# Optimization experiments

Measured on AMD Instinct MI355X. Metric: run time of the kernel, lower is better.

## Reference

```python
import jax, jax.numpy as jnp
import numpy as np

D_MODEL = 768; N_LAYER = 4; D_STATE = 64; D_CONV = 4; EXPAND = 2; HEADDIM = 64
D_INNER = EXPAND * D_MODEL          # 1536
NHEADS = D_INNER // HEADDIM         # 24
CONV_DIM = D_INNER + 2 * D_STATE    # 1664
D_IN_PROJ = 2 * D_INNER + 2 * D_STATE + NHEADS  # 3224
VOCAB = 50257; EPS = 1e-5


def _ln(x, w, b):
    m = x.mean(-1, keepdims=True)
    v = ((x - m) ** 2).mean(-1, keepdims=True)
    return (x - m) * jax.lax.rsqrt(v + EPS) * w + b


def _silu(x):
    return x * jax.nn.sigmoid(x)


def _mamba2(x, W_in, conv_w, conv_b, dt_bias, A_log, Dp, rms_w, W_out):
    # x: [B, L, d_model]
    Bsz, L, _ = x.shape
    zxbcdt = x @ W_in.T                                   # [B,L,D_IN_PROJ]
    z = zxbcdt[..., :D_INNER]
    xBC = zxbcdt[..., D_INNER:D_INNER + CONV_DIM]
    dt = zxbcdt[..., D_INNER + CONV_DIM:]                 # [B,L,H]
    # causal depthwise conv over time
    xc = jnp.transpose(xBC, (0, 2, 1))                    # [B,C,L]
    xc = jax.lax.conv_general_dilated(
        xc, conv_w[:, None, :], (1,), [(D_CONV - 1, 0)],
        dimension_numbers=('NCH', 'OIH', 'NCH'), feature_group_count=CONV_DIM)
    xBC = _silu(jnp.transpose(xc, (0, 2, 1)) + conv_b)
    xh = xBC[..., :D_INNER].reshape(Bsz, L, NHEADS, HEADDIM)
    Bc = xBC[..., D_INNER:D_INNER + D_STATE]              # [B,L,N]
    Cc = xBC[..., D_INNER + D_STATE:]                     # [B,L,N]
    dt = jax.nn.softplus(dt + dt_bias)                    # [B,L,H]
    dA = jnp.exp(dt * (-jnp.exp(A_log)))                  # [B,L,H]

    def step(h, inp):
        dA_t, dt_t, x_t, B_t, C_t = inp
        h = dA_t[:, :, None, None] * h + (dt_t[:, :, None] * x_t)[..., None] * B_t[:, None, None, :]
        return h, jnp.einsum('bhpn,bn->bhp', h, C_t)

    tm = lambda a: jnp.moveaxis(a, 1, 0)  # time-major
    h0 = jnp.zeros((Bsz, NHEADS, HEADDIM, D_STATE), x.dtype)
    _, y = jax.lax.scan(step, h0, (tm(dA), tm(dt), tm(xh), tm(Bc), tm(Cc)))
    y = jnp.moveaxis(y, 0, 1) + Dp[:, None] * xh          # [B,L,H,P]
    y = y.reshape(Bsz, L, D_INNER) * _silu(z)             # gate
    y = y * jax.lax.rsqrt((y * y).mean(-1, keepdims=True) + EPS) * rms_w
    return y @ W_out.T


def setup_inputs() -> dict:
    key = jax.random.key(0)
    ks = jax.random.split(key, 16)
    B, L = 1, 1024
    idx = jax.random.randint(ks[0], (B, L), 0, VOCAB)
    targets = jax.random.randint(ks[1], (B, L), 0, VOCAB)
    s = 0.02
    emb = jax.random.normal(ks[2], (VOCAB, D_MODEL), jnp.float32) * s
    ln_w = jnp.ones((N_LAYER, D_MODEL)); ln_b = jnp.zeros((N_LAYER, D_MODEL))
    W_in = jax.random.normal(ks[3], (N_LAYER, D_IN_PROJ, D_MODEL), jnp.float32) * s
    conv_w = jax.random.normal(ks[4], (N_LAYER, CONV_DIM, D_CONV), jnp.float32) * 0.1
    conv_b = jnp.zeros((N_LAYER, CONV_DIM))
    dt_bias = jnp.log(jnp.expm1(jax.random.uniform(ks[5], (N_LAYER, NHEADS), minval=0.001, maxval=0.1)))
    A_log = jnp.log(jax.random.uniform(ks[6], (N_LAYER, NHEADS), minval=1.0, maxval=16.0))
    Dp = jnp.ones((N_LAYER, NHEADS))
    rms_w = jnp.ones((N_LAYER, D_INNER))
    W_out = jax.random.normal(ks[7], (N_LAYER, D_MODEL, D_INNER), jnp.float32) * s
    lnf_w = jnp.ones((D_MODEL,)); lnf_b = jnp.zeros((D_MODEL,))
    return {"idx": idx, "targets": targets, "emb": emb, "ln_w": ln_w, "ln_b": ln_b,
            "W_in": W_in, "conv_w": conv_w, "conv_b": conv_b, "dt_bias": dt_bias,
            "A_log": A_log, "Dp": Dp, "rms_w": rms_w, "W_out": W_out,
            "lnf_w": lnf_w, "lnf_b": lnf_b}


def reference(idx, targets, emb, ln_w, ln_b, W_in, conv_w, conv_b, dt_bias,
              A_log, Dp, rms_w, W_out, lnf_w, lnf_b):
    x = emb[idx]                                          # [B,L,D]
    for i in range(N_LAYER):
        x = x + _mamba2(_ln(x, ln_w[i], ln_b[i]), W_in[i], conv_w[i], conv_b[i],
                        dt_bias[i], A_log[i], Dp[i], rms_w[i], W_out[i])
    x = _ln(x, lnf_w, lnf_b)
    logits = x @ emb.T                                    # tied head
    logp = jax.nn.log_softmax(logits, axis=-1)
    loss = -jnp.take_along_axis(logp, targets[..., None], axis=-1).mean()
    return logits, loss
```

## Files before the change

### kernel.cpp

```cpp
#include <hip/hip_runtime.h>
#include <hip/hip_bf16.h>
#include <math.h>

#define SL     1024
#define DMODEL 768
#define NLAYER 4
#define NSTATE 64
#define HEADDIM 64
#define DINNER 1536
#define NHEADS 24
#define CONVDIM 1664
#define DINPROJ 3224
#define VOCABN 50257

typedef __attribute__((ext_vector_type(8))) short short8;
typedef __attribute__((ext_vector_type(4))) short short4v;
typedef __attribute__((ext_vector_type(4))) float f32x4;

__device__ __forceinline__ short f2bf(float f) {
    unsigned int u = __builtin_bit_cast(unsigned int, f);
    u += 0x7fffu + ((u >> 16) & 1u);
    return (short)(u >> 16);
}

#define AS1 __attribute__((address_space(1)))
#define AS3 __attribute__((address_space(3)))
__device__ __forceinline__ void gl2lds16(const void* g, void* l) {
    __builtin_amdgcn_global_load_lds((const AS1 unsigned int*)g,
                                     (AS3 unsigned int*)(unsigned int)(uintptr_t)l,
                                     16, 0, 0);
}

template <int CTRL>
__device__ __forceinline__ float dppadd(float x) {
    int v = __builtin_amdgcn_update_dpp(0, __builtin_bit_cast(int, x), CTRL, 0xf, 0xf, true);
    return x + __builtin_bit_cast(float, v);
}

__global__ void cvt_k(const float* __restrict__ s, short* __restrict__ d, int n) {
    int i = (blockIdx.x * 256 + threadIdx.x) * 4;
    if (i >= n) return;
    float4 v = *(const float4*)(s + i);
    short4v o;
    o.x = f2bf(v.x); o.y = f2bf(v.y); o.z = f2bf(v.z); o.w = f2bf(v.w);
    *(short4v*)(d + i) = o;
}

__global__ void embed_k(const int* __restrict__ idx, const float* __restrict__ emb,
                        float* __restrict__ x) {
    int d = blockIdx.x * 256 + threadIdx.x;
    int t = blockIdx.y;
    x[t * DMODEL + d] = emb[(size_t)idx[t] * DMODEL + d];
}

__global__ void ln_k(const float* __restrict__ x, const float* __restrict__ w,
                     const float* __restrict__ b, short* __restrict__ out) {
    int row = blockIdx.x, t = threadIdx.x;
    const float* xr = x + row * DMODEL;
    float v0 = xr[t], v1 = xr[t + 256], v2 = xr[t + 512];
    float s = v0 + v1 + v2;
    float q = v0 * v0 + v1 * v1 + v2 * v2;
    __shared__ float sa[4], sb[4];
    for (int off = 32; off; off >>= 1) { s += __shfl_down(s, off); q += __shfl_down(q, off); }
    if (!(t & 63)) { sa[t >> 6] = s; sb[t >> 6] = q; }
    __syncthreads();
    s = sa[0] + sa[1] + sa[2] + sa[3];
    q = sb[0] + sb[1] + sb[2] + sb[3];
    float mean = s * (1.f / DMODEL);
    float var  = q * (1.f / DMODEL) - mean * mean;
    float rs = rsqrtf(var + 1e-5f);
    out[row * DMODEL + t      ] = f2bf((v0 - mean) * rs * w[t      ] + b[t      ]);
    out[row * DMODEL + t + 256] = f2bf((v1 - mean) * rs * w[t + 256] + b[t + 256]);
    out[row * DMODEL + t + 512] = f2bf((v2 - mean) * rs * w[t + 512] + b[t + 512]);
}

__global__ __launch_bounds__(256) void gemm_bb_k(const short* __restrict__ A,
                                                 const short* __restrict__ B,
                                                 float* __restrict__ C,
                                                 int N, int K, int addflag) {
    __shared__ __align__(16) short As[4096];
    __shared__ __align__(16) short Bs[4096];
    const int t = threadIdx.x;
    const int lane = t & 63, wv = t >> 6;

    const int nwg = gridDim.x;
    int bid = blockIdx.x;
    int qq = nwg >> 3, rr = nwg & 7;
    int xcd = bid & 7, ii = bid >> 3;
    int v = (xcd < rr ? xcd * (qq + 1) : rr * (qq + 1) + (xcd - rr) * qq) + ii;
    const int m0 = (v & 7) * 128;
    const int n0 = (v >> 3) * 128;

    const int wm = (wv >> 1) * 64, wn = (wv & 1) * 64;
    const int q4 = lane >> 4, l16 = lane & 15;

    f32x4 zero4 = {0.f, 0.f, 0.f, 0.f};
    f32x4 acc[4][4];
#pragma unroll
    for (int i = 0; i < 4; i++)
#pragma unroll
        for (int j = 0; j < 4; j++) acc[i][j] = zero4;

    for (int k0 = 0; k0 < K; k0 += 32) {
        __syncthreads();
#pragma unroll
        for (int i = 0; i < 2; i++) {
            int g = i * 256 + t;
            int q = g >> 7, r = g & 127;
            gl2lds16(A + (size_t)(m0 + r) * K + k0 + q * 8, As + g * 8);
        }
#pragma unroll
        for (int i = 0; i < 2; i++) {
            int g = i * 256 + t;
            int q = g >> 7, r = g & 127;
            int gr = n0 + r; if (gr > N - 1) gr = N - 1;
            gl2lds16(B + (size_t)gr * K + k0 + q * 8, Bs + g * 8);
        }
        __syncthreads();

        short8 af[4], bf[4];
#pragma unroll
        for (int mt = 0; mt < 4; mt++)
            af[mt] = *(const short8*)(As + q4 * 1024 + (wm + mt * 16 + l16) * 8);
#pragma unroll
        for (int nt = 0; nt < 4; nt++)
            bf[nt] = *(const short8*)(Bs + q4 * 1024 + (wn + nt * 16 + l16) * 8);
#pragma unroll
        for (int mt = 0; mt < 4; mt++)
#pragma unroll
            for (int nt = 0; nt < 4; nt++)
                acc[mt][nt] = __builtin_amdgcn_mfma_f32_16x16x32_bf16(af[mt], bf[nt], acc[mt][nt], 0, 0, 0);
    }

#pragma unroll
    for (int mt = 0; mt < 4; mt++) {
        int row = m0 + wm + mt * 16 + (lane >> 4) * 4;
#pragma unroll
        for (int nt = 0; nt < 4; nt++) {
            int col = n0 + wn + nt * 16 + l16;
            if (col < N) {
#pragma unroll
                for (int r = 0; r < 4; r++) {
                    size_t o = (size_t)(row + r) * N + col;
                    float val = acc[mt][nt][r];
                    if (addflag) C[o] += val; else C[o] = val;
                }
            }
        }
    }
}

__global__ __launch_bounds__(256) void gemm64_k(const short* __restrict__ A,
                                                const short* __restrict__ B,
                                                float* __restrict__ C,
                                                int N, int K, int addflag) {
    __shared__ __align__(16) short As[4096];
    __shared__ __align__(16) short Bs[4096];
    const int t = threadIdx.x;
    const int lane = t & 63, wv = t >> 6;
    const int m0 = blockIdx.x * 64, n0 = blockIdx.y * 64;
    const int wm = (wv >> 1) * 32, wn = (wv & 1) * 32;
    const int q4 = lane >> 4, l16 = lane & 15;

    f32x4 zero4 = {0.f, 0.f, 0.f, 0.f};
    f32x4 acc[2][2];
#pragma unroll
    for (int i = 0; i < 2; i++)
#pragma unroll
        for (int j = 0; j < 2; j++) acc[i][j] = zero4;

    for (int k0 = 0; k0 < K; k0 += 64) {
        __syncthreads();
#pragma unroll
        for (int i = 0; i < 2; i++) {
            int g = i * 256 + t;
            int q = g >> 6, r = g & 63;
            gl2lds16(A + (size_t)(m0 + r) * K + k0 + q * 8, As + g * 8);
        }
#pragma unroll
        for (int i = 0; i < 2; i++) {
            int g = i * 256 + t;
            int q = g >> 6, r = g & 63;
            int gr = n0 + r; if (gr > N - 1) gr = N - 1;
            gl2lds16(B + (size_t)gr * K + k0 + q * 8, Bs + g * 8);
        }
        __syncthreads();

#pragma unroll
        for (int kk = 0; kk < 2; kk++) {
            short8 af[2], bf[2];
#pragma unroll
            for (int mt = 0; mt < 2; mt++)
                af[mt] = *(const short8*)(As + (kk * 4 + q4) * 512 + (wm + mt * 16 + l16) * 8);
#pragma unroll
            for (int nt = 0; nt < 2; nt++)
                bf[nt] = *(const short8*)(Bs + (kk * 4 + q4) * 512 + (wn + nt * 16 + l16) * 8);
#pragma unroll
            for (int mt = 0; mt < 2; mt++)
#pragma unroll
                for (int nt = 0; nt < 2; nt++)
                    acc[mt][nt] = __builtin_amdgcn_mfma_f32_16x16x32_bf16(af[mt], bf[nt], acc[mt][nt], 0, 0, 0);
        }
    }

#pragma unroll
    for (int mt = 0; mt < 2; mt++) {
        int row = m0 + wm + mt * 16 + (lane >> 4) * 4;
#pragma unroll
        for (int nt = 0; nt < 2; nt++) {
            int col = n0 + wn + nt * 16 + l16;
            if (col < N) {
#pragma unroll
                for (int r = 0; r < 4; r++) {
                    size_t o = (size_t)(row + r) * N + col;
                    float val = acc[mt][nt][r];
                    if (addflag) C[o] += val; else C[o] = val;
                }
            }
        }
    }
}

#define LDSK 56
__global__ __launch_bounds__(256) void gemm_bt_k(const short* __restrict__ A,
                                                 const float* __restrict__ B,
                                                 float* __restrict__ C,
                                                 int N, int K, int addflag) {
    __shared__ __align__(16) short As[128 * LDSK];
    __shared__ __align__(16) short Bs[128 * LDSK];
    const int t = threadIdx.x;
    const int lane = t & 63, wv = t >> 6;
    const int m0 = blockIdx.x * 128, n0 = blockIdx.y * 128;
    const int wm = (wv >> 1) * 64, wn = (wv & 1) * 64;
    f32x4 zero4 = {0.f, 0.f, 0.f, 0.f};
    f32x4 acc[4][4];
#pragma unroll
    for (int i = 0; i < 4; i++)
#pragma unroll
        for (int j = 0; j < 4; j++) acc[i][j] = zero4;
    for (int k0 = 0; k0 < K; k0 += 32) {
        uint4  av[2];
        float4 bv[4];
#pragma unroll
        for (int i = 0; i < 2; i++) {
            int c = i * 256 + t, row = c >> 2, kc = c & 3;
            av[i] = *(const uint4*)(A + (size_t)(m0 + row) * K + k0 + kc * 8);
        }
#pragma unroll
        for (int i = 0; i < 4; i++) {
            int c = i * 256 + t, row = c >> 3, kc = c & 7;
            int gr = n0 + row; if (gr > N - 1) gr = N - 1;
            bv[i] = *(const float4*)(B + (size_t)gr * K + k0 + kc * 4);
        }
        __syncthreads();
#pragma unroll
        for (int i = 0; i < 2; i++) {
            int c = i * 256 + t, row = c >> 2, kc = c & 3;
            *(uint4*)(As + row * LDSK + kc * 8) = av[i];
        }
#pragma unroll
        for (int i = 0; i < 4; i++) {
            int c = i * 256 + t, row = c >> 3, kc = c & 7;
            short4v sv;
            sv.x = f2bf(bv[i].x); sv.y = f2bf(bv[i].y);
            sv.z = f2bf(bv[i].z); sv.w = f2bf(bv[i].w);
            *(short4v*)(Bs + row * LDSK + kc * 4) = sv;
        }
        __syncthreads();
        short8 af[4], bf[4];
#pragma unroll
        for (int mt = 0; mt < 4; mt++)
            af[mt] = *(const short8*)(As + (wm + mt * 16 + (lane & 15)) * LDSK + (lane >> 4) * 8);
#pragma unroll
        for (int nt = 0; nt < 4; nt++)
            bf[nt] = *(const short8*)(Bs + (wn + nt * 16 + (lane & 15)) * LDSK + (lane >> 4) * 8);
#pragma unroll
        for (int mt = 0; mt < 4; mt++)
#pragma unroll
            for (int nt = 0; nt < 4; nt++)
                acc[mt][nt] = __builtin_amdgcn_mfma_f32_16x16x32_bf16(af[mt], bf[nt], acc[mt][nt], 0, 0, 0);
    }
#pragma unroll
    for (int mt = 0; mt < 4; mt++) {
        int row = m0 + wm + mt * 16 + (lane >> 4) * 4;
#pragma unroll
        for (int nt = 0; nt < 4; nt++) {
            int col = n0 + wn + nt * 16 + (lane & 15);
            if (col < N) {
#pragma unroll
                for (int r = 0; r < 4; r++) {
                    size_t o = (size_t)(row + r) * N + col;
                    float val = acc[mt][nt][r];
                    if (addflag) C[o] += val; else C[o] = val;
                }
            }
        }
    }
}

__global__ void conv_k(const float* __restrict__ zx, const float* __restrict__ cw,
                       const float* __restrict__ cb, float* __restrict__ xbc) {
    int c = blockIdx.x * 256 + threadIdx.x;
    int t = blockIdx.y;
    if (c >= CONVDIM) return;
    float acc = cb[c];
#pragma unroll
    for (int j = 0; j < 4; j++) {
        int ts = t - 3 + j;
        if (ts >= 0) acc += cw[c * 4 + j] * zx[(size_t)ts * DINPROJ + DINNER + c];
    }
    xbc[(size_t)t * CONVDIM + c] = acc / (1.f + __expf(-acc));
}

__global__ void dt_k(const float* __restrict__ zx, const float* __restrict__ dt_bias,
                     const float* __restrict__ A_log, float* __restrict__ dts,
                     float* __restrict__ dAv) {
    int i = blockIdx.x * 256 + threadIdx.x;
    int tt = i / NHEADS, h = i % NHEADS;
    float d = zx[(size_t)tt * DINPROJ + 3200 + h] + dt_bias[h];
    float sp = (d > 20.f) ? d : log1pf(__expf(d));
    dts[i] = sp;
    dAv[i] = __expf(-__expf(A_log[h]) * sp);
}

__global__ __launch_bounds__(128) void scan_k(const float* __restrict__ xbc,
                                              const float* __restrict__ dts,
                                              const float* __restrict__ dAv,
                                              float* __restrict__ yraw) {
    __shared__ __align__(16) float BCs[64][128];
    __shared__ __align__(16) float xs[64][8];
    __shared__ float dash[64];
    int h = blockIdx.x >> 3;
    int pbase = (blockIdx.x & 7) * 8;
    int t = threadIdx.x, lane = t & 63, wv = t >> 6;
    int pl = wv * 4 + (lane >> 4);
    int n4 = lane & 15;
    float s0 = 0.f, s1 = 0.f, s2 = 0.f, s3 = 0.f;

    for (int tc = 0; tc < 16; tc++) {
        __syncthreads();
#pragma unroll 4
        for (int it = 0; it < 16; it++) {
            int idx = it * 128 + t;
            int trow = idx >> 5, c4 = idx & 31;
            *(float4*)&BCs[trow][c4 * 4] =
                *(const float4*)(xbc + (size_t)(tc * 64 + trow) * CONVDIM + DINNER + c4 * 4);
        }
        {
            int trow = t >> 1, hf = t & 1;
            float dtv = dts[(tc * 64 + trow) * NHEADS + h];
            float4 xv = *(const float4*)(xbc + (size_t)(tc * 64 + trow) * CONVDIM
                                         + h * HEADDIM + pbase + hf * 4);
            xv.x *= dtv; xv.y *= dtv; xv.z *= dtv; xv.w *= dtv;
            *(float4*)&xs[trow][hf * 4] = xv;
        }
        if (t < 64) dash[t] = dAv[(tc * 64 + t) * NHEADS + h];
        __syncthreads();

#pragma unroll 4
        for (int tt = 0; tt < 64; tt++) {
            float4 B4 = *(const float4*)&BCs[tt][n4 * 4];
            float4 C4 = *(const float4*)&BCs[tt][64 + n4 * 4];
            float dtx = xs[tt][pl];
            float da = dash[tt];
            s0 = fmaf(da, s0, dtx * B4.x);
            s1 = fmaf(da, s1, dtx * B4.y);
            s2 = fmaf(da, s2, dtx * B4.z);
            s3 = fmaf(da, s3, dtx * B4.w);
            float part = s0 * C4.x;
            part = fmaf(s1, C4.y, part);
            part = fmaf(s2, C4.z, part);
            part = fmaf(s3, C4.w, part);
            part = dppadd<0xB1>(part);
            part = dppadd<0x4E>(part);
            part = dppadd<0x114>(part);
            part = dppadd<0x118>(part);
            if (n4 == 0)
                yraw[(size_t)(tc * 64 + tt) * DINNER + h * HEADDIM + pbase + pl] = part;
        }
    }
}

__global__ void rms_k(const float* __restrict__ yraw, const float* __restrict__ zx,
                      const float* __restrict__ xbc, const float* __restrict__ Dp,
                      const float* __restrict__ rw, short* __restrict__ yn) {
    int row = blockIdx.x, t = threadIdx.x;
    float v[6];
    float q = 0.f;
#pragma unroll
    for (int j = 0; j < 6; j++) {
        int i = t + j * 256;
        float z  = zx[(size_t)row * DINPROJ + i];
        float xh = xbc[(size_t)row * CONVDIM + i];
        float y  = yraw[(size_t)row * DINNER + i] + Dp[i >> 6] * xh;
        float val = y * (z / (1.f + __expf(-z)));
        v[j] = val;
        q += val * val;
    }
    __shared__ float sb[4];
    for (int off = 32; off; off >>= 1) q += __shfl_down(q, off);
    if (!(t & 63)) sb[t >> 6] = q;
    __syncthreads();
    q = sb[0] + sb[1] + sb[2] + sb[3];
    float rs = rsqrtf(q * (1.f / DINNER) + 1e-5f);
#pragma unroll
    for (int j = 0; j < 6; j++) {
        int i = t + j * 256;
        yn[(size_t)row * DINNER + i] = f2bf(v[j] * rs * rw[i]);
    }
}

__global__ void loss_row_k(const float* __restrict__ logits, const int* __restrict__ tg,
                           float* __restrict__ lossp) {
    int r = blockIdx.x, t = threadIdx.x;
    const float* lr = logits + (size_t)r * VOCABN;
    float m = -3.0e38f, s = 0.f;
    for (int j = t; j < VOCABN; j += 256) {
        float v = lr[j];
        if (v > m) { s = s * __expf(m - v) + 1.f; m = v; }
        else s += __expf(v - m);
    }
    for (int off = 32; off; off >>= 1) {
        float mo = __shfl_down(m, off), so = __shfl_down(s, off);
        float nm = fmaxf(m, mo);
        s = s * __expf(m - nm) + so * __expf(mo - nm);
        m = nm;
    }
    __shared__ float sm[4], ss[4];
    if (!(t & 63)) { sm[t >> 6] = m; ss[t >> 6] = s; }
    __syncthreads();
    if (t == 0) {
        m = sm[0]; s = ss[0];
        for (int w = 1; w < 4; w++) {
            float nm = fmaxf(m, sm[w]);
            s = s * __expf(m - nm) + ss[w] * __expf(sm[w] - nm);
            m = nm;
        }
        lossp[r] = (m + logf(s)) - lr[tg[r]];
    }
}

__global__ void loss_fin_k(const float* __restrict__ lossp, float* __restrict__ out) {
    int t = threadIdx.x;
    float s = lossp[t] + lossp[t + 256] + lossp[t + 512] + lossp[t + 768];
    for (int off = 32; off; off >>= 1) s += __shfl_down(s, off);
    __shared__ float sb[4];
    if (!(t & 63)) sb[t >> 6] = s;
    __syncthreads();
    if (t == 0) out[(size_t)SL * VOCABN] = (sb[0] + sb[1] + sb[2] + sb[3]) * (1.f / SL);
}

extern "C" void kernel_launch(void* const* d_in, const int* in_sizes, int n_in,
                              void* d_out, int out_size, void* d_ws, size_t ws_size,
                              hipStream_t stream) {
    const int*   idx     = (const int*)d_in[0];
    const int*   targets = (const int*)d_in[1];
    const float* emb     = (const float*)d_in[2];
    const float* ln_w    = (const float*)d_in[3];
    const float* ln_b    = (const float*)d_in[4];
    const float* W_in    = (const float*)d_in[5];
    const float* conv_w  = (const float*)d_in[6];
    const float* conv_b  = (const float*)d_in[7];
    const float* dt_bias = (const float*)d_in[8];
    const float* A_log   = (const float*)d_in[9];
    const float* Dp      = (const float*)d_in[10];
    const float* rms_w   = (const float*)d_in[11];
    const float* W_out   = (const float*)d_in[12];
    const float* lnf_w   = (const float*)d_in[13];
    const float* lnf_b   = (const float*)d_in[14];

    char* ws = (char*)d_ws;
    float* x     = (float*)(ws + 0);
    short* xn    = (short*)(ws + 3145728);
    float* zx    = (float*)(ws + 4718592);
    float* xbc   = (float*)(ws + 17924096);
    float* dts   = (float*)(ws + 24739840);
    float* dAv   = (float*)(ws + 24838144);
    float* yraw  = (float*)(ws + 24936448);
    short* yn    = (short*)(ws + 31227904);
    float* lossp = (float*)(ws + 34373632);
    short* wInb  = (short*)(ws + 34377728);
    short* wOutb = (short*)(ws + 54183936);
    short* embb  = (short*)(ws + 63621120);
    float* logits = (float*)d_out;

    const bool big = ws_size >= 140815872ull;

    if (big) {
        int nWin  = NLAYER * DINPROJ * DMODEL;
        int nWout = NLAYER * DMODEL * DINNER;
        int nEmb  = VOCABN * DMODEL;
        cvt_k<<<(nWin / 4 + 255) / 256, 256, 0, stream>>>(W_in, wInb, nWin);
        cvt_k<<<(nWout / 4 + 255) / 256, 256, 0, stream>>>(W_out, wOutb, nWout);
        cvt_k<<<(nEmb / 4 + 255) / 256, 256, 0, stream>>>(emb, embb, nEmb);
    }

    embed_k<<<dim3(3, SL), 256, 0, stream>>>(idx, emb, x);
    for (int l = 0; l < NLAYER; l++) {
        ln_k<<<SL, 256, 0, stream>>>(x, ln_w + l * DMODEL, ln_b + l * DMODEL, xn);
        if (big)
            gemm64_k<<<dim3(16, 51), 256, 0, stream>>>(xn, wInb + (size_t)l * DINPROJ * DMODEL,
                                                       zx, DINPROJ, DMODEL, 0);
        else
            gemm_bt_k<<<dim3(8, 26), 256, 0, stream>>>(xn, W_in + (size_t)l * DINPROJ * DMODEL,
                                                       zx, DINPROJ, DMODEL, 0);
        conv_k<<<dim3(7, SL), 256, 0, stream>>>(zx, conv_w + l * CONVDIM * 4,
                                                conv_b + l * CONVDIM, xbc);
        dt_k<<<96, 256, 0, stream>>>(zx, dt_bias + l * NHEADS, A_log + l * NHEADS, dts, dAv);
        scan_k<<<192, 128, 0, stream>>>(xbc, dts, dAv, yraw);
        rms_k<<<SL, 256, 0, stream>>>(yraw, zx, xbc, Dp + l * NHEADS, rms_w + l * DINNER, yn);
        if (big)
            gemm64_k<<<dim3(16, 12), 256, 0, stream>>>(yn, wOutb + (size_t)l * DMODEL * DINNER,
                                                       x, DMODEL, DINNER, 1);
        else
            gemm_bt_k<<<dim3(8, 6), 256, 0, stream>>>(yn, W_out + (size_t)l * DMODEL * DINNER,
                                                      x, DMODEL, DINNER, 1);
    }
    ln_k<<<SL, 256, 0, stream>>>(x, lnf_w, lnf_b, xn);
    if (big)
        gemm_bb_k<<<8 * 393, 256, 0, stream>>>(xn, embb, logits, VOCABN, DMODEL, 0);
    else
        gemm_bt_k<<<dim3(8, 393), 256, 0, stream>>>(xn, emb, logits, VOCABN, DMODEL, 0);
    loss_row_k<<<SL, 256, 0, stream>>>(logits, targets, lossp);
    loss_fin_k<<<1, 256, 0, stream>>>(lossp, logits);
}
```

Measured before the change: 1.252 ms.

## Double-buffer LDS tiles in both GEMM kernels to overlap loads with MFMA

Both bf16 GEMM kernels now keep two LDS buffers and issue the global-to-LDS loads for the next K tile before computing the current one. Explicit vmcnt/lgkmcnt waits and raw s_barrier calls replace the two __syncthreads per iteration, so fragments are read into registers before a barrier and the MFMAs run while the next tile is in flight. This aims to hide global memory latency. In exchange it doubles LDS use, which may lower occupancy, and it depends on the hand-counted waitcnt values being correct.

```diff
diff --git a/kernel.cpp b/kernel.cpp
--- a/kernel.cpp
+++ b/kernel.cpp
@@ -78,8 +78,8 @@
                                                  const short* __restrict__ B,
                                                  float* __restrict__ C,
                                                  int N, int K, int addflag) {
-    __shared__ __align__(16) short As[4096];
-    __shared__ __align__(16) short Bs[4096];
+    __shared__ __align__(16) short As[2][4096];
+    __shared__ __align__(16) short Bs[2][4096];
     const int t = threadIdx.x;
     const int lane = t & 63, wv = t >> 6;
 
@@ -101,30 +101,44 @@
 #pragma unroll
         for (int j = 0; j < 4; j++) acc[i][j] = zero4;
 
-    for (int k0 = 0; k0 < K; k0 += 32) {
-        __syncthreads();
+    auto stage = [&](int buf, int k0) {
 #pragma unroll
         for (int i = 0; i < 2; i++) {
             int g = i * 256 + t;
             int q = g >> 7, r = g & 127;
-            gl2lds16(A + (size_t)(m0 + r) * K + k0 + q * 8, As + g * 8);
+            gl2lds16(A + (size_t)(m0 + r) * K + k0 + q * 8, &As[buf][g * 8]);
         }
 #pragma unroll
         for (int i = 0; i < 2; i++) {
             int g = i * 256 + t;
             int q = g >> 7, r = g & 127;
             int gr = n0 + r; if (gr > N - 1) gr = N - 1;
-            gl2lds16(B + (size_t)gr * K + k0 + q * 8, Bs + g * 8);
-        }
-        __syncthreads();
+            gl2lds16(B + (size_t)gr * K + k0 + q * 8, &Bs[buf][g * 8]);
+        }
+    };
+
+    const int NT = K >> 5;
+    stage(0, 0);
+    for (int tt = 0; tt < NT; tt++) {
+        const int cur = tt & 1;
+        if (tt + 1 < NT) {
+            stage(cur ^ 1, (tt + 1) << 5);
+            asm volatile("s_waitcnt vmcnt(4)" ::: "memory");
+        } else {
+            asm volatile("s_waitcnt vmcnt(0)" ::: "memory");
+        }
+        __builtin_amdgcn_s_barrier();
 
         short8 af[4], bf[4];
 #pragma unroll
         for (int mt = 0; mt < 4; mt++)
-            af[mt] = *(const short8*)(As + q4 * 1024 + (wm + mt * 16 + l16) * 8);
+            af[mt] = *(const short8*)(&As[cur][q4 * 1024 + (wm + mt * 16 + l16) * 8]);
 #pragma unroll
         for (int nt = 0; nt < 4; nt++)
-            bf[nt] = *(const short8*)(Bs + q4 * 1024 + (wn + nt * 16 + l16) * 8);
+            bf[nt] = *(const short8*)(&Bs[cur][q4 * 1024 + (wn + nt * 16 + l16) * 8]);
+        asm volatile("s_waitcnt lgkmcnt(0)" ::: "memory");
+        __builtin_amdgcn_s_barrier();
+
 #pragma unroll
         for (int mt = 0; mt < 4; mt++)
 #pragma unroll
@@ -154,8 +168,8 @@
                                                 const short* __restrict__ B,
                                                 float* __restrict__ C,
                                                 int N, int K, int addflag) {
-    __shared__ __align__(16) short As[4096];
-    __shared__ __align__(16) short Bs[4096];
+    __shared__ __align__(16) short As[2][4096];
+    __shared__ __align__(16) short Bs[2][4096];
     const int t = threadIdx.x;
     const int lane = t & 63, wv = t >> 6;
     const int m0 = blockIdx.x * 64, n0 = blockIdx.y * 64;
@@ -169,38 +183,54 @@
 #pragma unroll
         for (int j = 0; j < 2; j++) acc[i][j] = zero4;
 
-    for (int k0 = 0; k0 < K; k0 += 64) {
-        __syncthreads();
+    auto stage = [&](int buf, int k0) {
 #pragma unroll
         for (int i = 0; i < 2; i++) {
             int g = i * 256 + t;
             int q = g >> 6, r = g & 63;
-            gl2lds16(A + (size_t)(m0 + r) * K + k0 + q * 8, As + g * 8);
+            gl2lds16(A + (size_t)(m0 + r) * K + k0 + q * 8, &As[buf][g * 8]);
         }
 #pragma unroll
         for (int i = 0; i < 2; i++) {
             int g = i * 256 + t;
             int q = g >> 6, r = g & 63;
             int gr = n0 + r; if (gr > N - 1) gr = N - 1;
-            gl2lds16(B + (size_t)gr * K + k0 + q * 8, Bs + g * 8);
-        }
-        __syncthreads();
-
+            gl2lds16(B + (size_t)gr * K + k0 + q * 8, &Bs[buf][g * 8]);
+        }
+    };
+
+    const int NT = K >> 6;
+    stage(0, 0);
+    for (int tt = 0; tt < NT; tt++) {
+        const int cur = tt & 1;
+        if (tt + 1 < NT) {
+            stage(cur ^ 1, (tt + 1) << 6);
+            asm volatile("s_waitcnt vmcnt(4)" ::: "memory");
+        } else {
+            asm volatile("s_waitcnt vmcnt(0)" ::: "memory");
+        }
+        __builtin_amdgcn_s_barrier();
+
+        short8 af[2][2], bf[2][2];
 #pragma unroll
         for (int kk = 0; kk < 2; kk++) {
-            short8 af[2], bf[2];
 #pragma unroll
             for (int mt = 0; mt < 2; mt++)
-                af[mt] = *(const short8*)(As + (kk * 4 + q4) * 512 + (wm + mt * 16 + l16) * 8);
+                af[kk][mt] = *(const short8*)(&As[cur][(kk * 4 + q4) * 512 + (wm + mt * 16 + l16) * 8]);
 #pragma unroll
             for (int nt = 0; nt < 2; nt++)
-                bf[nt] = *(const short8*)(Bs + (kk * 4 + q4) * 512 + (wn + nt * 16 + l16) * 8);
+                bf[kk][nt] = *(const short8*)(&Bs[cur][(kk * 4 + q4) * 512 + (wn + nt * 16 + l16) * 8]);
+        }
+        asm volatile("s_waitcnt lgkmcnt(0)" ::: "memory");
+        __builtin_amdgcn_s_barrier();
+
+#pragma unroll
+        for (int kk = 0; kk < 2; kk++)
 #pragma unroll
             for (int mt = 0; mt < 2; mt++)
 #pragma unroll
                 for (int nt = 0; nt < 2; nt++)
-                    acc[mt][nt] = __builtin_amdgcn_mfma_f32_16x16x32_bf16(af[mt], bf[nt], acc[mt][nt], 0, 0, 0);
-        }
+                    acc[mt][nt] = __builtin_amdgcn_mfma_f32_16x16x32_bf16(af[kk][mt], bf[kk][nt], acc[mt][nt], 0, 0, 0);
     }
 
 #pragma unroll
```

Result: faster. 1.192 ms (-4.8%).
